# Kernel tuning notes

Measured on AMD Instinct MI355X. Metric: run time of the kernel, lower is better.

## Reference

```python
import jax, jax.numpy as jnp
import numpy as np

B, S_RAW, S_SUM, D_IN, H, NH = 32, 1024, 128, 300, 256, 4
DH = (2 * H) // NH  # per-head dim = 128


def _lstm_dir(x, Wih, Whh, b, reverse):
    """Single-direction LSTM (PyTorch gate order i,f,g,o). x: [B,S,D] -> [B,S,H]."""
    xg = jnp.einsum('bsd,gd->bsg', x, Wih) + b          # precompute input gates [B,S,4H]
    xg = jnp.swapaxes(xg, 0, 1)                          # [S,B,4H]
    Hh = Whh.shape[1]
    bsz = x.shape[0]

    def step(carry, g):
        h, c = carry
        gates = g + h @ Whh.T
        i, f, gg, o = jnp.split(gates, 4, axis=-1)
        c = jax.nn.sigmoid(f) * c + jax.nn.sigmoid(i) * jnp.tanh(gg)
        h = jax.nn.sigmoid(o) * jnp.tanh(c)
        return (h, c), h

    init = (jnp.zeros((bsz, Hh), x.dtype), jnp.zeros((bsz, Hh), x.dtype))
    _, hs = jax.lax.scan(step, init, xg, reverse=reverse)  # hs aligned with input time order
    return jnp.swapaxes(hs, 0, 1)


def _bilstm(x, pf, pb):
    return jnp.concatenate([_lstm_dir(x, *pf, False), _lstm_dir(x, *pb, True)], axis=-1)


def setup_inputs() -> dict:
    key = jax.random.key(0)
    ks = jax.random.split(key, 24)
    s_lstm = 1.0 / np.sqrt(H)
    s_proj = 1.0 / np.sqrt(2 * H)
    d = {}
    d['in_raw'] = jax.random.normal(ks[0], (B, S_RAW, D_IN), jnp.float32)
    d['in_sum'] = jax.random.normal(ks[1], (B, S_SUM, D_IN), jnp.float32)
    d['len_raw'] = jax.random.randint(ks[2], (B,), 0, S_RAW)
    d['len_sum'] = jax.random.randint(ks[3], (B,), 0, S_SUM)
    i = 4
    for name in ['raw_f', 'raw_b', 'sum_f', 'sum_b']:
        d[name + '_Wih'] = jax.random.uniform(ks[i], (4 * H, D_IN), jnp.float32, -s_lstm, s_lstm); i += 1
        d[name + '_Whh'] = jax.random.uniform(ks[i], (4 * H, H), jnp.float32, -s_lstm, s_lstm); i += 1
        d[name + '_b'] = jax.random.uniform(ks[i], (4 * H,), jnp.float32, -s_lstm, s_lstm); i += 1
    d['Wq'] = jax.random.uniform(ks[i], (NH, 2 * H, DH), jnp.float32, -s_proj, s_proj); i += 1
    d['Wk'] = jax.random.uniform(ks[i], (NH, 2 * H, DH), jnp.float32, -s_proj, s_proj); i += 1
    d['Wv'] = jax.random.uniform(ks[i], (NH, 2 * H, DH), jnp.float32, -s_proj, s_proj)
    return d


def reference(in_raw, in_sum, len_raw, len_sum,
              raw_f_Wih, raw_f_Whh, raw_f_b, raw_b_Wih, raw_b_Whh, raw_b_b,
              sum_f_Wih, sum_f_Whh, sum_f_b, sum_b_Wih, sum_b_Whh, sum_b_b,
              Wq, Wk, Wv):
    # BiLSTM encoders (dropout is identity in eval mode)
    out_raw = _bilstm(in_raw, (raw_f_Wih, raw_f_Whh, raw_f_b), (raw_b_Wih, raw_b_Whh, raw_b_b))  # [B,Sr,2H]
    out_sum = _bilstm(in_sum, (sum_f_Wih, sum_f_Whh, sum_f_b), (sum_b_Wih, sum_b_Whh, sum_b_b))  # [B,Ss,2H]

    # mean_pooling over the first len_sum[i] timesteps (lengths clamped to >=1)
    lens = jnp.maximum(len_sum, 1)
    mask = (jnp.arange(S_SUM)[None, :] < lens[:, None]).astype(out_sum.dtype)  # [B,Ss]
    sum_vec = jnp.einsum('bsd,bs->bd', out_sum, mask) / lens.astype(out_sum.dtype)[:, None]  # [B,2H]

    # per-head cross-attention against the single pooled summary vector (rank-1 attention)
    q = jnp.einsum('bsd,hde->hbse', out_raw, Wq)   # [NH,B,Sr,DH]
    k = jnp.einsum('bd,hde->hbe', sum_vec, Wk)     # [NH,B,DH]
    v = jnp.einsum('bd,hde->hbe', sum_vec, Wv)     # [NH,B,DH]
    scores = jnp.einsum('hbse,hbe->hbs', q, k)     # [NH,B,Sr] (use_divide_dk=False)
    attn = jax.nn.softmax(scores, axis=-1)
    rst = attn[..., None] * v[:, :, None, :] + q   # outer product + residual, [NH,B,Sr,DH]

    # concat heads along last dim -> [B,Sr,2H]
    rst = jnp.transpose(rst, (1, 2, 0, 3)).reshape(B, S_RAW, NH * DH)
    return rst
```

## Files before the change

kernel.cpp:

```cpp
#include <hip/hip_runtime.h>

typedef _Float16 f16;
typedef _Float16 half2t __attribute__((ext_vector_type(2)));
typedef _Float16 half8 __attribute__((ext_vector_type(8)));
typedef float f32x4 __attribute__((ext_vector_type(4)));

#define KP 320
#define DIN 300
#define SRAW 1024
#define SSUM 128

static constexpr size_t OFF_XG_RAW  = 0;
static constexpr size_t OFF_XG_SUM  = OFF_XG_RAW + (size_t)2*32*1024*1024*2;
static constexpr size_t OFF_OUT_RAW = OFF_XG_SUM + (size_t)2*32*128*1024*2;
static constexpr size_t OFF_OUT_SUM = OFF_OUT_RAW + (size_t)32*1024*512*2;
static constexpr size_t OFF_A_RAW   = OFF_OUT_SUM + (size_t)32*128*512*2;
static constexpr size_t OFF_A_SUM   = OFF_A_RAW + (size_t)32768*KP*2;
static constexpr size_t OFF_BIH_RAW = OFF_A_SUM + (size_t)4096*KP*2;
static constexpr size_t OFF_BIH_SUM = OFF_BIH_RAW + (size_t)2048*KP*2;
static constexpr size_t OFF_WHH     = OFF_BIH_SUM + (size_t)2048*KP*2;
static constexpr size_t OFF_WQ      = OFF_WHH + (size_t)4*64*512*8*2;
static constexpr size_t OFF_KB      = OFF_WQ + (size_t)512*512*2;
static constexpr size_t OFF_VB      = OFF_KB + (size_t)4*32*128*4;
static constexpr size_t OFF_ATTN    = OFF_VB + (size_t)4*32*128*4;
static constexpr size_t WS_NEED     = OFF_ATTN + (size_t)4*32*1024*4;

__global__ void pack_kernel(
    const float* __restrict__ in_raw, const float* __restrict__ in_sum,
    const float* __restrict__ wih_rf, const float* __restrict__ wih_rb,
    const float* __restrict__ wih_sf, const float* __restrict__ wih_sb,
    const float* __restrict__ whh_rf, const float* __restrict__ whh_rb,
    const float* __restrict__ whh_sf, const float* __restrict__ whh_sb,
    const float* __restrict__ wq,
    f16* __restrict__ a_raw, f16* __restrict__ a_sum,
    f16* __restrict__ bih_raw, f16* __restrict__ bih_sum,
    f16* __restrict__ whh16, f16* __restrict__ wq16)
{
  constexpr size_t N1 = (size_t)32768*KP;
  constexpr size_t N2 = (size_t)4096*KP;
  constexpr size_t N3 = (size_t)2048*KP;
  constexpr size_t N5 = (size_t)4*64*512*8;
  constexpr size_t N6 = (size_t)512*512;
  const size_t TOT = N1+N2+N3+N3+N5+N6;
  const size_t stride = (size_t)gridDim.x*blockDim.x;
  for (size_t i = (size_t)blockIdx.x*blockDim.x + threadIdx.x; i < TOT; i += stride) {
    size_t j = i;
    if (j < N1) {
      size_t m = j/KP, k = j - m*KP;
      a_raw[j] = (f16)(k < DIN ? in_raw[m*DIN + k] : 0.f);
      continue;
    }
    j -= N1;
    if (j < N2) {
      size_t m = j/KP, k = j - m*KP;
      a_sum[j] = (f16)(k < DIN ? in_sum[m*DIN + k] : 0.f);
      continue;
    }
    j -= N2;
    if (j < N3) {
      size_t n = j/KP, k = j - n*KP;
      float v = 0.f;
      if (k < DIN) v = (n < 1024) ? wih_rf[n*DIN + k] : wih_rb[(n-1024)*DIN + k];
      bih_raw[j] = (f16)v;
      continue;
    }
    j -= N3;
    if (j < N3) {
      size_t n = j/KP, k = j - n*KP;
      float v = 0.f;
      if (k < DIN) v = (n < 1024) ? wih_sf[n*DIN + k] : wih_sb[(n-1024)*DIN + k];
      bih_sum[j] = (f16)v;
      continue;
    }
    j -= N3;
    if (j < N5) {
      int ed = (int)(j >> 18);
      int c  = (int)((j >> 12) & 63);
      int t  = (int)((j >> 3) & 511);
      int ii = (int)(j & 7);
      int jrow = c >> 2, q = c & 3;
      int rg = t >> 3, ks = t & 7;
      int row = rg*16 + jrow;
      int col = ks*32 + q*8 + ii;
      const float* src = (ed==0)?whh_rf:(ed==1)?whh_rb:(ed==2)?whh_sf:whh_sb;
      whh16[j] = (f16)src[(size_t)row*256 + col];
      continue;
    }
    j -= N5;
    {
      int n = (int)(j >> 9), k = (int)(j & 511);
      int h = n >> 7, dh = n & 127;
      wq16[j] = (f16)wq[((size_t)h*512 + k)*128 + dh];
    }
  }
}

template<int EPI>
__global__ __launch_bounds__(256) void gemm_kernel(
    const f16* __restrict__ A, const f16* __restrict__ Bm,
    float* __restrict__ Cf, f16* __restrict__ Cx,
    const float* __restrict__ bias0, const float* __restrict__ bias1,
    int K, int ldcN, size_t dirStride)
{
  __shared__ __align__(16) f16 As[128*40];
  __shared__ __align__(16) f16 Bs[128*40];
  const int tid = threadIdx.x;
  const int m0 = blockIdx.x*128, n0 = blockIdx.y*128;
  const int w = tid >> 6, lane = tid & 63;
  const int wm = w >> 1, wn = w & 1;
  const int lr = lane & 15, lk = lane >> 4;
  f32x4 acc[4][4] = {};
  const int nsteps = K >> 5;
  for (int kt = 0; kt < nsteps; ++kt) {
    __syncthreads();
    #pragma unroll
    for (int it = 0; it < 2; ++it) {
      int c = tid + it*256;
      int r = c >> 2, kc = c & 3;
      *(uint4*)&As[r*40 + kc*8] = *(const uint4*)&A[(size_t)(m0+r)*K + kt*32 + kc*8];
      *(uint4*)&Bs[r*40 + kc*8] = *(const uint4*)&Bm[(size_t)(n0+r)*K + kt*32 + kc*8];
    }
    __syncthreads();
    half8 af[4], bf[4];
    #pragma unroll
    for (int mt = 0; mt < 4; ++mt) af[mt] = *(const half8*)&As[(wm*64 + mt*16 + lr)*40 + lk*8];
    #pragma unroll
    for (int nt = 0; nt < 4; ++nt) bf[nt] = *(const half8*)&Bs[(wn*64 + nt*16 + lr)*40 + lk*8];
    #pragma unroll
    for (int mt = 0; mt < 4; ++mt)
      #pragma unroll
      for (int nt = 0; nt < 4; ++nt)
        acc[mt][nt] = __builtin_amdgcn_mfma_f32_16x16x32_f16(af[mt], bf[nt], acc[mt][nt], 0, 0, 0);
  }
  const int rb = lk*4;
  #pragma unroll
  for (int mt = 0; mt < 4; ++mt) {
    #pragma unroll
    for (int nt = 0; nt < 4; ++nt) {
      int n = n0 + wn*64 + nt*16 + lr;
      int mloc = m0 + wm*64 + mt*16 + rb;
      if (EPI == 0) {
        #pragma unroll
        for (int r = 0; r < 4; ++r)
          Cf[(size_t)(mloc+r)*ldcN + n] = acc[mt][nt][r];
      } else {
        int dir = n >> 10, cc = n & 1023;
        int gate = cc >> 8, u = cc & 255;
        float bs = (dir ? bias1 : bias0)[cc];
        f16* dst = Cx + (size_t)dir*dirStride;
        #pragma unroll
        for (int r = 0; r < 4; ++r)
          dst[(size_t)(mloc+r)*1024 + u*4 + gate] = (f16)(acc[mt][nt][r] + bs);
      }
    }
  }
}

#define RROWS 13
#define LROWS 3

__device__ __forceinline__ float dot8(float acc, uint4 wv, uint4 hv) {
#if __has_builtin(__builtin_amdgcn_fdot2)
  union { uint4 u; half2t h[4]; } W, Hh;
  W.u = wv; Hh.u = hv;
  #pragma unroll
  for (int i = 0; i < 4; ++i) acc = __builtin_amdgcn_fdot2(W.h[i], Hh.h[i], acc, false);
#else
  union { uint4 u; f16 h[8]; } W, Hh;
  W.u = wv; Hh.u = hv;
  #pragma unroll
  for (int i = 0; i < 8; ++i) acc += (float)W.h[i]*(float)Hh.h[i];
#endif
  return acc;
}

__device__ __forceinline__ float sigmoid_f(float x) {
  float e = __expf(-x);
  return __builtin_amdgcn_rcpf(1.f + e);
}
__device__ __forceinline__ float tanh_f(float x) {
  float e = __expf(2.f * x);
  return 1.f - 2.f * __builtin_amdgcn_rcpf(e + 1.f);
}

__device__ __forceinline__ void pin4(uint4& v) {
  asm volatile("" : "+v"(v.x), "+v"(v.y), "+v"(v.z), "+v"(v.w));
}

template<int CTRL>
__device__ __forceinline__ float dpp_add(float v) {
  int m = __builtin_amdgcn_update_dpp(0, __builtin_bit_cast(int, v), CTRL, 0xf, 0xf, true);
  return v + __builtin_bit_cast(float, m);
}
__device__ __forceinline__ float reduce8(float v) {
  v = dpp_add<0xB1>(v);
  v = dpp_add<0x4E>(v);
  v = dpp_add<0x141>(v);
  return v;
}

__global__ void __launch_bounds__(512) __attribute__((amdgpu_waves_per_eu(2, 2)))
lstm_kernel(
    const f16* __restrict__ whh16,
    const f16* __restrict__ xg_raw, const f16* __restrict__ xg_sum,
    f16* __restrict__ out_raw, f16* __restrict__ out_sum)
{
  const int wg = blockIdx.x;
  const int e = wg >> 6, r2 = wg & 63, d = r2 >> 5, b = r2 & 31;
  const int S = e ? SSUM : SRAW;
  const int t = threadIdx.x;
  const int rg = t >> 3, ks = t & 7;
  const uint4* wb = (const uint4*)(whh16 + (size_t)(e*2+d)*(64*512*8));
  const f16* xg = (e ? xg_sum : xg_raw) + ((size_t)(d*32 + b))*(size_t)S*1024;
  f16* outp = (e ? out_sum : out_raw) + (size_t)b*S*512 + d*256;

  __shared__ __align__(16) uint4 wl[LROWS*4*512];
  __shared__ float pre[1024];
  __shared__ __align__(16) f16 hrep[4*264];

  #pragma unroll
  for (int c = 0; c < LROWS*4; ++c) wl[c*512 + t] = wb[(RROWS*4 + c)*512 + t];
  uint4 wr[RROWS*4];
  #pragma unroll
  for (int c = 0; c < RROWS*4; ++c) wr[c] = wb[c*512 + t];
  #pragma unroll
  for (int c = 0; c < RROWS*4; ++c) pin4(wr[c]);

  if (t < 256) {
    #pragma unroll
    for (int cpy = 0; cpy < 4; ++cpy) hrep[cpy*264 + t] = (f16)0.f;
  }
  float cst = 0.f;
  const int hbyte = (ks >> 1)*528 + ks*64;
  const int preS = ((rg >> 4) << 8) + ((rg & 15) << 4);
  __syncthreads();

  for (int st = 0; st < S; ++st) {
    const int s = d ? (S - 1 - st) : st;

    uint2 xq;
    if (t < 256) xq = *(const uint2*)(xg + ((size_t)s*1024 + t*4));

    uint4 hv[4];
    #pragma unroll
    for (int q = 0; q < 4; ++q)
      hv[q] = *(const uint4*)((const char*)hrep + hbyte + q*16);

    float pa = 0.f, pb = 0.f;

    #pragma unroll
    for (int j = 0; j < RROWS; ++j) {
      float rs = 0.f;
      #pragma unroll
      for (int q = 0; q < 4; ++q) rs = dot8(rs, wr[j*4 + q], hv[q]);
      rs = reduce8(rs);
      if (j < 8) { pa = (ks == j) ? rs : pa; }
      else       { pb = (ks == j - 8) ? rs : pb; }
    }
    #pragma unroll
    for (int j = 0; j < LROWS; ++j) {
      float rs = 0.f;
      #pragma unroll
      for (int q = 0; q < 4; ++q) rs = dot8(rs, wl[(j*4 + q)*512 + t], hv[q]);
      rs = reduce8(rs);
      pb = (ks == 5 + j) ? rs : pb;
    }

    pre[preS + ks]     = pa;
    pre[preS + 8 + ks] = pb;
    __syncthreads();

    if (t < 256) {
      half2t x01 = __builtin_bit_cast(half2t, xq.x);
      half2t x23 = __builtin_bit_cast(half2t, xq.y);
      float vi = pre[t]       + (float)x01[0];
      float vf = pre[256 + t] + (float)x01[1];
      float vg = pre[512 + t] + (float)x23[0];
      float vo = pre[768 + t] + (float)x23[1];
      float ig = sigmoid_f(vi);
      float fg = sigmoid_f(vf);
      float gg = tanh_f(vg);
      float og = sigmoid_f(vo);
      cst = fg*cst + ig*gg;
      float hval = og*tanh_f(cst);
      f16 hf = (f16)hval;
      #pragma unroll
      for (int cpy = 0; cpy < 4; ++cpy) hrep[cpy*264 + t] = hf;
      outp[(size_t)s*512 + t] = hf;
    }
    __syncthreads();
  }
}

__global__ __launch_bounds__(256) void pool_kv_kernel(
    const f16* __restrict__ out_sum, const int* __restrict__ len_sum,
    const float* __restrict__ Wk, const float* __restrict__ Wv,
    float* __restrict__ kb, float* __restrict__ vb)
{
  const int b = blockIdx.x, t = threadIdx.x;
  __shared__ float sv[512];
  int len = len_sum[b]; if (len < 1) len = 1;
  float a0 = 0.f, a1 = 0.f;
  for (int s = 0; s < len; ++s) {
    const f16* row = out_sum + ((size_t)b*SSUM + s)*512;
    a0 += (float)row[t];
    a1 += (float)row[t+256];
  }
  float inv = 1.f/(float)len;
  sv[t] = a0*inv; sv[t+256] = a1*inv;
  __syncthreads();
  #pragma unroll
  for (int half = 0; half < 2; ++half) {
    int o = t + half*256;
    int h = o >> 7, dh = o & 127;
    const float* wkp = Wk + (size_t)h*512*128 + dh;
    const float* wvp = Wv + (size_t)h*512*128 + dh;
    float ak = 0.f, av = 0.f;
    for (int e2 = 0; e2 < 512; ++e2) {
      float sve = sv[e2];
      ak += sve*wkp[(size_t)e2*128];
      av += sve*wvp[(size_t)e2*128];
    }
    kb[((size_t)h*32 + b)*128 + dh] = ak;
    vb[((size_t)h*32 + b)*128 + dh] = av;
  }
}

__global__ __launch_bounds__(256) void attn_kernel(
    const float* __restrict__ q, const float* __restrict__ kb, float* __restrict__ attn)
{
  const int hb = blockIdx.x;
  const int h = hb >> 5, b = hb & 31;
  const int t = threadIdx.x;
  __shared__ __align__(16) float kk[128];
  __shared__ float red[4];
  if (t < 128) kk[t] = kb[(size_t)hb*128 + t];
  __syncthreads();
  float vals[4];
  #pragma unroll
  for (int i = 0; i < 4; ++i) {
    int s = t + i*256;
    const float4* qp = (const float4*)(q + ((size_t)b*1024 + s)*512 + h*128);
    const float4* kp = (const float4*)kk;
    float a = 0.f;
    #pragma unroll
    for (int e2 = 0; e2 < 32; ++e2) {
      float4 qq = qp[e2], kx = kp[e2];
      a += qq.x*kx.x + qq.y*kx.y + qq.z*kx.z + qq.w*kx.w;
    }
    vals[i] = a;
  }
  float m = fmaxf(fmaxf(vals[0], vals[1]), fmaxf(vals[2], vals[3]));
  for (int o = 1; o < 64; o <<= 1) m = fmaxf(m, __shfl_xor(m, o));
  if ((t & 63) == 0) red[t >> 6] = m;
  __syncthreads();
  m = fmaxf(fmaxf(red[0], red[1]), fmaxf(red[2], red[3]));
  __syncthreads();
  float ex[4], lsum = 0.f;
  #pragma unroll
  for (int i = 0; i < 4; ++i) { ex[i] = __expf(vals[i] - m); lsum += ex[i]; }
  for (int o = 1; o < 64; o <<= 1) lsum += __shfl_xor(lsum, o);
  if ((t & 63) == 0) red[t >> 6] = lsum;
  __syncthreads();
  float inv = 1.f/(red[0] + red[1] + red[2] + red[3]);
  #pragma unroll
  for (int i = 0; i < 4; ++i) attn[(size_t)hb*1024 + t + i*256] = ex[i]*inv;
}

__global__ __launch_bounds__(256) void final_kernel(
    float* __restrict__ out, const float* __restrict__ attn, const float* __restrict__ vb)
{
  const size_t TOT4 = (size_t)32*1024*512/4;
  const size_t stride = (size_t)gridDim.x*blockDim.x;
  for (size_t i = (size_t)blockIdx.x*blockDim.x + threadIdx.x; i < TOT4; i += stride) {
    int c4 = (int)(i & 127);
    int h = c4 >> 5;
    size_t srow = i >> 7;
    int b = (int)(srow >> 10), s = (int)(srow & 1023);
    float a = attn[((size_t)h*32 + b)*1024 + s];
    float4 vv = ((const float4*)vb)[((size_t)h*32 + b)*32 + (c4 & 31)];
    float4 qq = ((float4*)out)[i];
    qq.x += a*vv.x; qq.y += a*vv.y; qq.z += a*vv.z; qq.w += a*vv.w;
    ((float4*)out)[i] = qq;
  }
}

extern "C" void kernel_launch(void* const* d_in, const int* in_sizes, int n_in,
                              void* d_out, int out_size, void* d_ws, size_t ws_size,
                              hipStream_t stream)
{
  const float* in_raw = (const float*)d_in[0];
  const float* in_sum = (const float*)d_in[1];
  const int*  len_sum = (const int*)d_in[3];
  const float* rf_wih = (const float*)d_in[4];
  const float* rf_whh = (const float*)d_in[5];
  const float* rf_b   = (const float*)d_in[6];
  const float* rb_wih = (const float*)d_in[7];
  const float* rb_whh = (const float*)d_in[8];
  const float* rb_b   = (const float*)d_in[9];
  const float* sf_wih = (const float*)d_in[10];
  const float* sf_whh = (const float*)d_in[11];
  const float* sf_b   = (const float*)d_in[12];
  const float* sb_wih = (const float*)d_in[13];
  const float* sb_whh = (const float*)d_in[14];
  const float* sb_b   = (const float*)d_in[15];
  const float* wq     = (const float*)d_in[16];
  const float* wk     = (const float*)d_in[17];
  const float* wv     = (const float*)d_in[18];

  if (ws_size < WS_NEED) return;

  char* ws = (char*)d_ws;
  f16* xg_raw_p  = (f16*)(ws + OFF_XG_RAW);
  f16* xg_sum_p  = (f16*)(ws + OFF_XG_SUM);
  f16* out_raw_p = (f16*)(ws + OFF_OUT_RAW);
  f16* out_sum_p = (f16*)(ws + OFF_OUT_SUM);
  f16* a_raw_p   = (f16*)(ws + OFF_A_RAW);
  f16* a_sum_p   = (f16*)(ws + OFF_A_SUM);
  f16* bih_raw_p = (f16*)(ws + OFF_BIH_RAW);
  f16* bih_sum_p = (f16*)(ws + OFF_BIH_SUM);
  f16* whh16_p   = (f16*)(ws + OFF_WHH);
  f16* wq16_p    = (f16*)(ws + OFF_WQ);
  float* kb_p    = (float*)(ws + OFF_KB);
  float* vb_p    = (float*)(ws + OFF_VB);
  float* attn_p  = (float*)(ws + OFF_ATTN);
  float* qout    = (float*)d_out;

  pack_kernel<<<4096, 256, 0, stream>>>(
      in_raw, in_sum, rf_wih, rb_wih, sf_wih, sb_wih,
      rf_whh, rb_whh, sf_whh, sb_whh, wq,
      a_raw_p, a_sum_p, bih_raw_p, bih_sum_p, whh16_p, wq16_p);

  gemm_kernel<1><<<dim3(256, 16), 256, 0, stream>>>(
      a_raw_p, bih_raw_p, nullptr, xg_raw_p, rf_b, rb_b, KP, 0, (size_t)32*1024*1024);
  gemm_kernel<1><<<dim3(32, 16), 256, 0, stream>>>(
      a_sum_p, bih_sum_p, nullptr, xg_sum_p, sf_b, sb_b, KP, 0, (size_t)32*128*1024);

  lstm_kernel<<<128, 512, 0, stream>>>(whh16_p, xg_raw_p, xg_sum_p, out_raw_p, out_sum_p);

  gemm_kernel<0><<<dim3(256, 4), 256, 0, stream>>>(
      out_raw_p, wq16_p, qout, nullptr, nullptr, nullptr, 512, 512, 0);

  pool_kv_kernel<<<32, 256, 0, stream>>>(out_sum_p, len_sum, wk, wv, kb_p, vb_p);
  attn_kernel<<<128, 256, 0, stream>>>(qout, kb_p, attn_p);
  final_kernel<<<4096, 256, 0, stream>>>(qout, attn_p, vb_p);
}
```

Before: 2.045 ms.

## Move gate activations into all threads and rebalance register/LDS weight rows

The input-gate GEMM epilogue now stores gates in natural order instead of interleaved per unit. In the LSTM step, every one of the 512 threads adds its own xg value and applies sigmoid/tanh to its two pre-activations before writing to shared memory. This spreads the four gate activations per unit over all threads instead of serialising them in the first 256, shortening the critical path after the barrier. It also moves one more Whh row from LDS to registers (14/2) and adds a min-blocks launch bound, which increases register pressure and risks spills.

```diff
diff --git a/kernel.cpp b/kernel.cpp
--- a/kernel.cpp
+++ b/kernel.cpp
@@ -145,19 +145,18 @@
           Cf[(size_t)(mloc+r)*ldcN + n] = acc[mt][nt][r];
       } else {
         int dir = n >> 10, cc = n & 1023;
-        int gate = cc >> 8, u = cc & 255;
         float bs = (dir ? bias1 : bias0)[cc];
         f16* dst = Cx + (size_t)dir*dirStride;
         #pragma unroll
         for (int r = 0; r < 4; ++r)
-          dst[(size_t)(mloc+r)*1024 + u*4 + gate] = (f16)(acc[mt][nt][r] + bs);
+          dst[(size_t)(mloc+r)*1024 + cc] = (f16)(acc[mt][nt][r] + bs);
       }
     }
   }
 }
 
-#define RROWS 13
-#define LROWS 3
+#define RROWS 14
+#define LROWS 2
 
 __device__ __forceinline__ float dot8(float acc, uint4 wv, uint4 hv) {
 #if __has_builtin(__builtin_amdgcn_fdot2)
@@ -199,7 +198,7 @@
   return v;
 }
 
-__global__ void __launch_bounds__(512) __attribute__((amdgpu_waves_per_eu(2, 2)))
+__global__ void __launch_bounds__(512, 2) __attribute__((amdgpu_waves_per_eu(2, 2)))
 lstm_kernel(
     const f16* __restrict__ whh16,
     const f16* __restrict__ xg_raw, const f16* __restrict__ xg_sum,
@@ -232,14 +231,17 @@
   }
   float cst = 0.f;
   const int hbyte = (ks >> 1)*528 + ks*64;
-  const int preS = ((rg >> 4) << 8) + ((rg & 15) << 4);
+  const int gate = rg >> 4;
+  const int preS = (gate << 8) + ((rg & 15) << 4);
+  const int ua = (gate << 8) + ((rg & 15) << 4) + ks;
+  const bool isG = (gate == 2);
   __syncthreads();
 
   for (int st = 0; st < S; ++st) {
     const int s = d ? (S - 1 - st) : st;
 
-    uint2 xq;
-    if (t < 256) xq = *(const uint2*)(xg + ((size_t)s*1024 + t*4));
+    float xva = (float)xg[(size_t)s*1024 + ua];
+    float xvb = (float)xg[(size_t)s*1024 + ua + 8];
 
     uint4 hv[4];
     #pragma unroll
@@ -263,24 +265,19 @@
       #pragma unroll
       for (int q = 0; q < 4; ++q) rs = dot8(rs, wl[(j*4 + q)*512 + t], hv[q]);
       rs = reduce8(rs);
-      pb = (ks == 5 + j) ? rs : pb;
-    }
-
-    pre[preS + ks]     = pa;
-    pre[preS + 8 + ks] = pb;
+      pb = (ks == 6 + j) ? rs : pb;
+    }
+
+    float va = pa + xva, vb = pb + xvb;
+    float aa, ab;
+    if (isG) { aa = tanh_f(va);    ab = tanh_f(vb);    }
+    else     { aa = sigmoid_f(va); ab = sigmoid_f(vb); }
+    pre[preS + ks]     = aa;
+    pre[preS + 8 + ks] = ab;
     __syncthreads();
 
     if (t < 256) {
-      half2t x01 = __builtin_bit_cast(half2t, xq.x);
-      half2t x23 = __builtin_bit_cast(half2t, xq.y);
-      float vi = pre[t]       + (float)x01[0];
-      float vf = pre[256 + t] + (float)x01[1];
-      float vg = pre[512 + t] + (float)x23[0];
-      float vo = pre[768 + t] + (float)x23[1];
-      float ig = sigmoid_f(vi);
-      float fg = sigmoid_f(vf);
-      float gg = tanh_f(vg);
-      float og = sigmoid_f(vo);
+      float ig = pre[t], fg = pre[256 + t], gg = pre[512 + t], og = pre[768 + t];
       cst = fg*cst + ig*gg;
       float hval = og*tanh_f(cst);
       f16 hf = (f16)hval;
```

New measurement: 2.204 ms. 1.08x slower.

## Merge input-gate GEMMs into one launch and fuse softmax with residual update

Applied to the files above, without the earlier changes.

The two input-projection GEMMs (raw and summary) become a single launch whose grid covers both problems, so one launch replaces two. The attention softmax kernel and the final outer-product residual kernel are fused: attention weights stay in shared memory and each block updates its own head/batch slice of q in place. The separate attn buffer and the final_kernel's full grid-stride pass go away. In exchange the fused kernel runs only 128 blocks for the final update, which may use the GPU less fully than the previous 4096-block launch. The LSTM launch attribute is also rewritten as launch_bounds(512,2).

```diff
diff --git a/kernel.cpp b/kernel.cpp
--- a/kernel.cpp
+++ b/kernel.cpp
@@ -95,12 +95,9 @@
   }
 }
 
-template<int EPI>
 __global__ __launch_bounds__(256) void gemm_kernel(
     const f16* __restrict__ A, const f16* __restrict__ Bm,
-    float* __restrict__ Cf, f16* __restrict__ Cx,
-    const float* __restrict__ bias0, const float* __restrict__ bias1,
-    int K, int ldcN, size_t dirStride)
+    float* __restrict__ Cf, int K, int ldcN)
 {
   __shared__ __align__(16) f16 As[128*40];
   __shared__ __align__(16) f16 Bs[128*40];
@@ -139,19 +136,72 @@
     for (int nt = 0; nt < 4; ++nt) {
       int n = n0 + wn*64 + nt*16 + lr;
       int mloc = m0 + wm*64 + mt*16 + rb;
-      if (EPI == 0) {
-        #pragma unroll
-        for (int r = 0; r < 4; ++r)
-          Cf[(size_t)(mloc+r)*ldcN + n] = acc[mt][nt][r];
-      } else {
-        int dir = n >> 10, cc = n & 1023;
-        int gate = cc >> 8, u = cc & 255;
-        float bs = (dir ? bias1 : bias0)[cc];
-        f16* dst = Cx + (size_t)dir*dirStride;
-        #pragma unroll
-        for (int r = 0; r < 4; ++r)
-          dst[(size_t)(mloc+r)*1024 + u*4 + gate] = (f16)(acc[mt][nt][r] + bs);
-      }
+      #pragma unroll
+      for (int r = 0; r < 4; ++r)
+        Cf[(size_t)(mloc+r)*ldcN + n] = acc[mt][nt][r];
+    }
+  }
+}
+
+__global__ __launch_bounds__(256) void gemm_dual_kernel(
+    const f16* __restrict__ A1, const f16* __restrict__ B1,
+    const f16* __restrict__ A2, const f16* __restrict__ B2,
+    f16* __restrict__ C1, f16* __restrict__ C2,
+    const float* __restrict__ b1f, const float* __restrict__ b1b,
+    const float* __restrict__ b2f, const float* __restrict__ b2b)
+{
+  __shared__ __align__(16) f16 As[128*40];
+  __shared__ __align__(16) f16 Bs[128*40];
+  const bool second = (blockIdx.x >= 256);
+  const f16* A  = second ? A2 : A1;
+  const f16* Bm = second ? B2 : B1;
+  f16* Cx       = second ? C2 : C1;
+  const float* bias0 = second ? b2f : b1f;
+  const float* bias1 = second ? b2b : b1b;
+  const size_t dirStride = second ? (size_t)32*128*1024 : (size_t)32*1024*1024;
+  const int m0 = (second ? ((int)blockIdx.x - 256) : (int)blockIdx.x)*128;
+  const int n0 = blockIdx.y*128;
+  const int tid = threadIdx.x;
+  const int w = tid >> 6, lane = tid & 63;
+  const int wm = w >> 1, wn = w & 1;
+  const int lr = lane & 15, lk = lane >> 4;
+  f32x4 acc[4][4] = {};
+  const int nsteps = KP >> 5;
+  for (int kt = 0; kt < nsteps; ++kt) {
+    __syncthreads();
+    #pragma unroll
+    for (int it = 0; it < 2; ++it) {
+      int c = tid + it*256;
+      int r = c >> 2, kc = c & 3;
+      *(uint4*)&As[r*40 + kc*8] = *(const uint4*)&A[(size_t)(m0+r)*KP + kt*32 + kc*8];
+      *(uint4*)&Bs[r*40 + kc*8] = *(const uint4*)&Bm[(size_t)(n0+r)*KP + kt*32 + kc*8];
+    }
+    __syncthreads();
+    half8 af[4], bf[4];
+    #pragma unroll
+    for (int mt = 0; mt < 4; ++mt) af[mt] = *(const half8*)&As[(wm*64 + mt*16 + lr)*40 + lk*8];
+    #pragma unroll
+    for (int nt = 0; nt < 4; ++nt) bf[nt] = *(const half8*)&Bs[(wn*64 + nt*16 + lr)*40 + lk*8];
+    #pragma unroll
+    for (int mt = 0; mt < 4; ++mt)
+      #pragma unroll
+      for (int nt = 0; nt < 4; ++nt)
+        acc[mt][nt] = __builtin_amdgcn_mfma_f32_16x16x32_f16(af[mt], bf[nt], acc[mt][nt], 0, 0, 0);
+  }
+  const int rb = lk*4;
+  #pragma unroll
+  for (int mt = 0; mt < 4; ++mt) {
+    #pragma unroll
+    for (int nt = 0; nt < 4; ++nt) {
+      int n = n0 + wn*64 + nt*16 + lr;
+      int mloc = m0 + wm*64 + mt*16 + rb;
+      int dir = n >> 10, cc = n & 1023;
+      int gate = cc >> 8, u = cc & 255;
+      float bs = (dir ? bias1 : bias0)[cc];
+      f16* dst = Cx + (size_t)dir*dirStride;
+      #pragma unroll
+      for (int r = 0; r < 4; ++r)
+        dst[(size_t)(mloc+r)*1024 + u*4 + gate] = (f16)(acc[mt][nt][r] + bs);
     }
   }
 }
@@ -199,8 +249,7 @@
   return v;
 }
 
-__global__ void __launch_bounds__(512) __attribute__((amdgpu_waves_per_eu(2, 2)))
-lstm_kernel(
+__global__ __launch_bounds__(512, 2) void lstm_kernel(
     const f16* __restrict__ whh16,
     const f16* __restrict__ xg_raw, const f16* __restrict__ xg_sum,
     f16* __restrict__ out_raw, f16* __restrict__ out_sum)
@@ -326,15 +375,18 @@
   }
 }
 
-__global__ __launch_bounds__(256) void attn_kernel(
-    const float* __restrict__ q, const float* __restrict__ kb, float* __restrict__ attn)
+__global__ __launch_bounds__(256) void attn_final_kernel(
+    float* __restrict__ q, const float* __restrict__ kb, const float* __restrict__ vb)
 {
   const int hb = blockIdx.x;
   const int h = hb >> 5, b = hb & 31;
   const int t = threadIdx.x;
   __shared__ __align__(16) float kk[128];
+  __shared__ __align__(16) float vvs[128];
+  __shared__ float att[1024];
   __shared__ float red[4];
   if (t < 128) kk[t] = kb[(size_t)hb*128 + t];
+  else if (t < 256) vvs[t - 128] = vb[(size_t)hb*128 + (t - 128)];
   __syncthreads();
   float vals[4];
   #pragma unroll
@@ -364,24 +416,18 @@
   __syncthreads();
   float inv = 1.f/(red[0] + red[1] + red[2] + red[3]);
   #pragma unroll
-  for (int i = 0; i < 4; ++i) attn[(size_t)hb*1024 + t + i*256] = ex[i]*inv;
-}
-
-__global__ __launch_bounds__(256) void final_kernel(
-    float* __restrict__ out, const float* __restrict__ attn, const float* __restrict__ vb)
-{
-  const size_t TOT4 = (size_t)32*1024*512/4;
-  const size_t stride = (size_t)gridDim.x*blockDim.x;
-  for (size_t i = (size_t)blockIdx.x*blockDim.x + threadIdx.x; i < TOT4; i += stride) {
-    int c4 = (int)(i & 127);
-    int h = c4 >> 5;
-    size_t srow = i >> 7;
-    int b = (int)(srow >> 10), s = (int)(srow & 1023);
-    float a = attn[((size_t)h*32 + b)*1024 + s];
-    float4 vv = ((const float4*)vb)[((size_t)h*32 + b)*32 + (c4 & 31)];
-    float4 qq = ((float4*)out)[i];
-    qq.x += a*vv.x; qq.y += a*vv.y; qq.z += a*vv.z; qq.w += a*vv.w;
-    ((float4*)out)[i] = qq;
+  for (int i = 0; i < 4; ++i) att[t + i*256] = ex[i]*inv;
+  __syncthreads();
+
+  const int sg = t >> 5, f4 = t & 31;
+  const float4 vv4 = ((const float4*)vvs)[f4];
+  for (int chunk = 0; chunk < 128; ++chunk) {
+    int s = chunk*8 + sg;
+    float a = att[s];
+    float4* qp = (float4*)(q + ((size_t)b*1024 + s)*512 + h*128);
+    float4 qq = qp[f4];
+    qq.x += a*vv4.x; qq.y += a*vv4.y; qq.z += a*vv4.z; qq.w += a*vv4.w;
+    qp[f4] = qq;
   }
 }
 
@@ -423,7 +469,6 @@
   f16* wq16_p    = (f16*)(ws + OFF_WQ);
   float* kb_p    = (float*)(ws + OFF_KB);
   float* vb_p    = (float*)(ws + OFF_VB);
-  float* attn_p  = (float*)(ws + OFF_ATTN);
   float* qout    = (float*)d_out;
 
   pack_kernel<<<4096, 256, 0, stream>>>(
@@ -431,17 +476,15 @@
       rf_whh, rb_whh, sf_whh, sb_whh, wq,
       a_raw_p, a_sum_p, bih_raw_p, bih_sum_p, whh16_p, wq16_p);
 
-  gemm_kernel<1><<<dim3(256, 16), 256, 0, stream>>>(
-      a_raw_p, bih_raw_p, nullptr, xg_raw_p, rf_b, rb_b, KP, 0, (size_t)32*1024*1024);
-  gemm_kernel<1><<<dim3(32, 16), 256, 0, stream>>>(
-      a_sum_p, bih_sum_p, nullptr, xg_sum_p, sf_b, sb_b, KP, 0, (size_t)32*128*1024);
+  gemm_dual_kernel<<<dim3(288, 16), 256, 0, stream>>>(
+      a_raw_p, bih_raw_p, a_sum_p, bih_sum_p,
+      xg_raw_p, xg_sum_p, rf_b, rb_b, sf_b, sb_b);
 
   lstm_kernel<<<128, 512, 0, stream>>>(whh16_p, xg_raw_p, xg_sum_p, out_raw_p, out_sum_p);
 
-  gemm_kernel<0><<<dim3(256, 4), 256, 0, stream>>>(
-      out_raw_p, wq16_p, qout, nullptr, nullptr, nullptr, 512, 512, 0);
+  gemm_kernel<<<dim3(256, 4), 256, 0, stream>>>(
+      out_raw_p, wq16_p, qout, 512, 512);
 
   pool_kv_kernel<<<32, 256, 0, stream>>>(out_sum_p, len_sum, wk, wv, kb_p, vb_p);
-  attn_kernel<<<128, 256, 0, stream>>>(qout, kb_p, attn_p);
-  final_kernel<<<4096, 256, 0, stream>>>(qout, attn_p, vb_p);
-}
+  attn_final_kernel<<<128, 256, 0, stream>>>(qout, kb_p, vb_p);
+}
```

Result: no change. 2.072 ms (+1.3%).
